# Kernel optimization log

Measured on AMD Instinct MI355X. Metric: run time of the kernel, lower is better.

Reference implementation:

```python
import jax, jax.numpy as jnp
import numpy as np

B, C, P, H, W, S = 4, 256, 128, 56, 56, 5
EPS = 1e-5


def setup_inputs() -> dict:
    key = jax.random.key(0)
    ks = jax.random.split(key, 6)
    return {
        "x": jax.random.normal(ks[0], (B, C, H, W), jnp.float32),
        "Wt": jax.random.normal(ks[1], (P, C), jnp.float32) * 0.05,
        "Wp": jax.random.normal(ks[2], (P, C), jnp.float32) * 0.05,
        "Wg": jax.random.normal(ks[3], (S, P, C), jnp.float32) * 0.05,
        "W1": jax.random.normal(ks[4], (S, C, P), jnp.float32) * 0.05,
        "W2": jax.random.normal(ks[5], (S, C, P), jnp.float32) * 0.05,
        "gamma": jnp.ones((S, C), jnp.float32),
        "beta": jnp.zeros((S, C), jnp.float32),
    }


def _batchnorm(o, g, b):
    # training-mode BN over (batch, spatial); o: [b, C, n]
    mean = o.mean(axis=(0, 2), keepdims=True)
    var = ((o - mean) ** 2).mean(axis=(0, 2), keepdims=True)
    return (o - mean) * jax.lax.rsqrt(var + EPS) * g[None, :, None] + b[None, :, None]


def reference(x, Wt, Wp, Wg, W1, W2, gamma, beta):
    b, c, h, w = x.shape
    n = h * w
    xf = x.reshape(b, c, n)
    # 1x1 conv projections == channel matmuls
    t = jax.nn.relu(jnp.einsum('pc,bcn->bpn', Wt, xf))  # is_norm branch uses relu
    p = jax.nn.relu(jnp.einsum('pc,bcn->bpn', Wp, xf))
    att = jnp.einsum('bpi,bpj->bij', t, p)              # [b, n, n] affinity
    att = 0.5 * (att + jnp.swapaxes(att, 1, 2))         # is_sys symmetrization
    d = att.sum(axis=2)                                  # degree [b, n]
    d_safe = jnp.where(d != 0, d, 1.0)
    d_inv = jnp.where(d != 0, jax.lax.rsqrt(d_safe), 0.0)
    att = att * d_inv[:, None, :] * d_inv[:, :, None]    # D^-1/2 A D^-1/2
    out = xf
    for s in range(S):  # fixed small stage count
        g = jnp.einsum('pc,bcn->bpn', Wg[s], out)        # [b, P, n]
        ag = jnp.einsum('bij,bpj->bpi', att, g)          # att @ g over spatial
        o = jnp.einsum('cp,bpn->bcn', W1[s], ag) + jnp.einsum('cp,bpn->bcn', W2[s], g)
        out = _batchnorm(o, gamma[s], beta[s]) + out     # BN + residual
    return out.reshape(b, c, h, w)
```

## Files before the change

kernel.cpp:

```cpp
#include <hip/hip_runtime.h>

#define VMC(n) asm volatile("s_waitcnt vmcnt(" #n ")" ::: "memory")

namespace {

constexpr int Bc = 4;
constexpr int Cc = 256;
constexpr int Pc = 128;
constexpr int NcT = 3136;
constexpr int Np = 3200;
constexpr int Sc = 5;
constexpr int KSn = 5;
constexpr int KCH = 640;
constexpr float EPSc = 1e-5f;

typedef __attribute__((ext_vector_type(8))) short bf16x8;
typedef __attribute__((ext_vector_type(4))) float f32x4;
typedef __attribute__((ext_vector_type(8))) unsigned short u16x8;
typedef __attribute__((ext_vector_type(4))) unsigned short u16x4;

__device__ inline float bf2f(unsigned short u) {
    return __uint_as_float(((unsigned)u) << 16);
}
__device__ inline unsigned short f2bf(float f) {
    unsigned u = __float_as_uint(f);
    return (unsigned short)((u + 0x7FFFu + ((u >> 16) & 1u)) >> 16);
}

struct GP {
    const unsigned short* A; int lda; long aB; long aSl;
    const unsigned short* Bw; int ldb; long bB; long bSl;
    const unsigned short* A2; int lda2; long aB2;
    const unsigned short* B2; int ldb2; long bB2;
    int K; int K2; int nsl; int kchunk;
    unsigned short* outSM; int ldsm; long smB; long smSlice;
    unsigned short* outCM; long cmB;
    float* ps; float* ps2;
    const float* bnsc; const float* bnsh;
    const float* dinv;
    const unsigned short* oin;
    float* resid;
};

template <int MT, int EPI, int CMOUT, bool SPLITK, int BNSTAT, bool FUSEBN,
          bool XORM, bool DUALK>
__global__ __launch_bounds__(256) void mgemm(GP p)
{
    constexpr int TBA = MT * 64 * 2;
    constexpr int TBB = 128 * 64 * 2;
    constexpr int BUF = TBA + TBB;
    constexpr int OTB = MT * 132 * 4;
    constexpr int LDSZ = (4 * BUF > OTB + 2048) ? 4 * BUF : (OTB + 2048);
    __shared__ __align__(16) char lds[LDSZ];

    int b, kstart;
    long smOff;
    if (SPLITK) {
        b = blockIdx.z & 3;
        int ks = blockIdx.z >> 2;
        kstart = ks * p.kchunk;
        smOff = (long)ks * p.smSlice;
    } else {
        b = blockIdx.z; kstart = 0; smOff = 0;
    }
    const int n0 = blockIdx.x * 128;
    const int m0 = blockIdx.y * MT;
    const int tid = threadIdx.x;
    const int w = tid >> 6, l = tid & 63;

    const unsigned short* Ab = p.A + (size_t)b * p.aB + (size_t)m0 * p.lda;
    const unsigned short* Bb = p.Bw + (size_t)b * p.bB + (size_t)n0 * p.ldb;

    const int srow8 = tid >> 3;
    const int sgran = tid & 7;
    const int sswz = (sgran ^ (srow8 & 7)) * 8;
    constexpr int AR = MT / 32;

    constexpr int WC = (MT == 128) ? 2 : 4;
    constexpr int NB = 128 / WC / 16;
    const int wr = w / WC, wc = w % WC;

    f32x4 acc[4][NB] = {};
    float fup[AR][8];

    auto stage1 = [&](int buf, int sl, int k0) {
        char* base = lds + buf * BUF;
        const unsigned short* As = Ab + (size_t)sl * p.aSl + k0 + sswz;
#pragma unroll
        for (int j = 0; j < AR; ++j)
            __builtin_amdgcn_global_load_lds(
                (const __attribute__((address_space(1))) void*)
                    (As + (size_t)(j * 32 + srow8) * p.lda),
                (__attribute__((address_space(3))) void*)(base + j * 4096 + tid * 16),
                16, 0, 0);
        const unsigned short* Bs = Bb + (size_t)sl * p.bSl + k0 + sswz;
#pragma unroll
        for (int j = 0; j < 4; ++j)
            __builtin_amdgcn_global_load_lds(
                (const __attribute__((address_space(1))) void*)
                    (Bs + (size_t)(j * 32 + srow8) * p.ldb),
                (__attribute__((address_space(3))) void*)(base + TBA + j * 4096 + tid * 16),
                16, 0, 0);
    };

    auto stageB1 = [&](int buf, int k0) {
        char* base = lds + buf * BUF + TBA;
        const unsigned short* Bs = Bb + k0 + sswz;
#pragma unroll
        for (int j = 0; j < 4; ++j)
            __builtin_amdgcn_global_load_lds(
                (const __attribute__((address_space(1))) void*)
                    (Bs + (size_t)(j * 32 + srow8) * p.ldb),
                (__attribute__((address_space(3))) void*)(base + j * 4096 + tid * 16),
                16, 0, 0);
    };

    auto fbLoad = [&](int k0) {
        const float* scp = p.bnsc + k0 + sgran * 8;
        const float* shp = p.bnsh + k0 + sgran * 8;
        float4 s0 = *(const float4*)scp, s1 = *(const float4*)(scp + 4);
        float4 h0 = *(const float4*)shp, h1 = *(const float4*)(shp + 4);
#pragma unroll
        for (int j = 0; j < AR; ++j) {
            int row = j * 32 + srow8;
            int n = m0 + row;
            size_t off = ((size_t)b * Np + n) * 256 + k0 + sgran * 8;
            if (n < NcT) {
                u16x8 ov = *(const u16x8*)(p.oin + off);
                float4 r0 = *(const float4*)(p.resid + off);
                float4 r1 = *(const float4*)(p.resid + off + 4);
                fup[j][0] = r0.x + fmaf(bf2f(ov[0]), s0.x, h0.x);
                fup[j][1] = r0.y + fmaf(bf2f(ov[1]), s0.y, h0.y);
                fup[j][2] = r0.z + fmaf(bf2f(ov[2]), s0.z, h0.z);
                fup[j][3] = r0.w + fmaf(bf2f(ov[3]), s0.w, h0.w);
                fup[j][4] = r1.x + fmaf(bf2f(ov[4]), s1.x, h1.x);
                fup[j][5] = r1.y + fmaf(bf2f(ov[5]), s1.y, h1.y);
                fup[j][6] = r1.z + fmaf(bf2f(ov[6]), s1.z, h1.z);
                fup[j][7] = r1.w + fmaf(bf2f(ov[7]), s1.w, h1.w);
                float4 w0, w1;
                w0.x = fup[j][0]; w0.y = fup[j][1]; w0.z = fup[j][2]; w0.w = fup[j][3];
                w1.x = fup[j][4]; w1.y = fup[j][5]; w1.z = fup[j][6]; w1.w = fup[j][7];
                *(float4*)(p.resid + off) = w0;
                *(float4*)(p.resid + off + 4) = w1;
            } else {
#pragma unroll
                for (int i = 0; i < 8; ++i) fup[j][i] = 0.f;
            }
        }
    };
    auto fbWrite = [&](int buf) {
        char* base = lds + buf * BUF;
#pragma unroll
        for (int j = 0; j < AR; ++j) {
            int row = j * 32 + srow8;
            u16x8 hv;
#pragma unroll
            for (int i = 0; i < 8; ++i) hv[i] = f2bf(fup[j][i]);
            *(u16x8*)(base + row * 128 + ((sgran ^ (row & 7)) << 4)) = hv;
        }
    };

    auto compute = [&](int buf) {
        const char* base = lds + buf * BUF;
        const int lo = l & 15, gq = l >> 4;
#pragma unroll
        for (int kh = 0; kh < 2; ++kh) {
            const int lg = kh * 4 + gq;
            bf16x8 bf[NB];
#pragma unroll
            for (int c = 0; c < NB; ++c) {
                int brow = wc * (16 * NB) + c * 16 + lo;
                bf[c] = *(const bf16x8*)(base + TBA + brow * 128 +
                                         ((lg ^ (brow & 7)) << 4));
            }
#pragma unroll
            for (int r = 0; r < 4; ++r) {
                int arow = wr * 64 + r * 16 + lo;
                bf16x8 af = *(const bf16x8*)(base + arow * 128 +
                                             ((lg ^ (arow & 7)) << 4));
#pragma unroll
                for (int c = 0; c < NB; ++c)
                    acc[r][c] = __builtin_amdgcn_mfma_f32_16x16x32_bf16(
                        af, bf[c], acc[r][c], 0, 0, 0);
            }
        }
    };

    if constexpr (FUSEBN) {
        const int nst = p.K >> 6;
        fbLoad(kstart);
        fbWrite(0);
        stageB1(0, kstart);
        __syncthreads();
        for (int s = 0; s < nst; ++s) {
            if (s + 1 < nst) {
                fbLoad(kstart + ((s + 1) << 6));
                stageB1((s + 1) & 1, kstart + ((s + 1) << 6));
            }
            compute(s & 1);
            if (s + 1 < nst) fbWrite((s + 1) & 1);
            __syncthreads();
        }
    } else {
        const int nsteps1 = (SPLITK ? p.kchunk : p.K) >> 6;
        const int spl2 = DUALK ? (p.K2 >> 6) : 0;
        const int loop1 = p.nsl * nsteps1;
        const int tot = loop1 + spl2;

        const unsigned short* Ab2 = DUALK ?
            (p.A2 + (size_t)b * p.aB2 + (size_t)m0 * p.lda2) : nullptr;
        const unsigned short* Bb2 = DUALK ?
            (p.B2 + (size_t)b * p.bB2 + (size_t)n0 * p.ldb2) : nullptr;
        auto stage2 = [&](int buf, int k0) {
            if constexpr (DUALK) {
                char* base = lds + buf * BUF;
                const unsigned short* As = Ab2 + k0 + sswz;
#pragma unroll
                for (int j = 0; j < AR; ++j)
                    __builtin_amdgcn_global_load_lds(
                        (const __attribute__((address_space(1))) void*)
                            (As + (size_t)(j * 32 + srow8) * p.lda2),
                        (__attribute__((address_space(3))) void*)(base + j * 4096 + tid * 16),
                        16, 0, 0);
                const unsigned short* Bs = Bb2 + k0 + sswz;
#pragma unroll
                for (int j = 0; j < 4; ++j)
                    __builtin_amdgcn_global_load_lds(
                        (const __attribute__((address_space(1))) void*)
                            (Bs + (size_t)(j * 32 + srow8) * p.ldb2),
                        (__attribute__((address_space(3))) void*)(base + TBA + j * 4096 + tid * 16),
                        16, 0, 0);
            }
        };

        auto stage_g = [&](int buf, int g) {
            if (g < loop1) {
                int sl = g / nsteps1;
                int st = g - sl * nsteps1;
                stage1(buf, sl, kstart + (st << 6));
            } else {
                stage2(buf, (g - loop1) << 6);
            }
        };

        stage_g(0, 0);
        if (1 < tot) stage_g(1, 1);
        if (2 < tot) stage_g(2, 2);
        for (int gs = 0; gs < tot; ++gs) {
            if constexpr (MT == 64) {
                if (gs + 2 < tot) VMC(12);
                else if (gs + 1 < tot) VMC(6);
                else VMC(0);
            } else {
                if (gs + 2 < tot) VMC(16);
                else if (gs + 1 < tot) VMC(8);
                else VMC(0);
            }
            __builtin_amdgcn_s_barrier();
            __builtin_amdgcn_sched_barrier(0);
            if (gs + 3 < tot) stage_g((gs + 3) & 3, gs + 3);
            compute(gs & 3);
        }
        __syncthreads();
    }

    float* ot = (float*)lds;
    {
        const int lo = l & 15, gq = l >> 4;
#pragma unroll
        for (int r = 0; r < 4; ++r)
#pragma unroll
            for (int c = 0; c < NB; ++c)
#pragma unroll
                for (int j = 0; j < 4; ++j) {
                    float v = acc[r][c][j];
                    if (EPI == 1) v = fmaxf(v, 0.f);
                    ot[(wr * 64 + r * 16 + gq * 4 + j) * 132 +
                       wc * (16 * NB) + c * 16 + lo] = v;
                }
    }
    __syncthreads();

    {
        constexpr int TPR = 256 / MT;
        const int r = tid / TPR;
        const int c0 = (tid % TPR) * (MT / 2);
        const int m0s = XORM ? (m0 ^ 128) : m0;
        unsigned short* dst = p.outSM + (size_t)b * p.smB + smOff +
                              (size_t)(m0s + r) * p.ldsm + n0 + c0;
#pragma unroll
        for (int k = 0; k < MT / 16; ++k) {
            u16x8 o;
#pragma unroll
            for (int j = 0; j < 8; ++j) o[j] = f2bf(ot[r * 132 + c0 + 8 * k + j]);
            *(u16x8*)(dst + 8 * k) = o;
        }
    }

    if (CMOUT) {
        const int c = tid >> 1, r0 = (tid & 1) * (MT / 2);
        const float* dv = p.dinv + (size_t)b * Np + m0 + r0;
        unsigned short* dst = p.outCM + (size_t)b * p.cmB +
                              (size_t)(n0 + c) * Np + m0 + r0;
#pragma unroll
        for (int k = 0; k < MT / 16; ++k) {
            u16x8 o;
#pragma unroll
            for (int j = 0; j < 8; ++j) {
                float v = ot[(r0 + 8 * k + j) * 132 + c];
                if (CMOUT == 2) v *= dv[8 * k + j];
                o[j] = f2bf(v);
            }
            *(u16x8*)(dst + 8 * k) = o;
        }
    }

    if (BNSTAT) {
        float* p1 = (float*)(lds + OTB);
        float* p2 = p1 + 256;
        const int col = tid & 127, half = tid >> 7;
        float s = 0.f, s2 = 0.f;
#pragma unroll
        for (int i = 0; i < MT / 2; ++i) {
            float v = ot[(half * (MT / 2) + i) * 132 + col];
            s += v;
            if (BNSTAT == 2) s2 = fmaf(v, v, s2);
        }
        p1[half * 128 + col] = s;
        if (BNSTAT == 2) p2[half * 128 + col] = s2;
        __syncthreads();
        if (tid < 128) {
            float aa = p1[tid] + p1[128 + tid];
            size_t slot = ((size_t)b * gridDim.y + blockIdx.y) * 256 + n0 + tid;
            p.ps[slot] = aa;
            if (BNSTAT == 2) p.ps2[slot] = p2[tid] + p2[128 + tid];
        }
    }
}

__global__ __launch_bounds__(256) void prep_k(
    const float* __restrict__ x, const float* __restrict__ Wt,
    const float* __restrict__ Wp, const float* __restrict__ Wg,
    const float* __restrict__ W1, const float* __restrict__ W2,
    unsigned short* __restrict__ Wcomb, unsigned short* __restrict__ Wgh,
    unsigned short* __restrict__ W1h, unsigned short* __restrict__ W2h,
    float* __restrict__ out_sm, unsigned short* __restrict__ outh)
{
    __shared__ float tb[64][65];
    int item = blockIdx.x;
    int t = threadIdx.x;
    if (item < 544) {
        size_t e = ((size_t)item * 256 + t) * 4;
        const float* src; unsigned short* dst;
        if (e < 32768)       { src = Wt + e;           dst = Wcomb + e; }
        else if (e < 65536)  { src = Wp + (e - 32768); dst = Wcomb + e; }
        else if (e < 229376) { size_t o = e - 65536;  src = Wg + o; dst = Wgh + o; }
        else if (e < 393216) { size_t o = e - 229376; src = W1 + o; dst = W1h + o; }
        else                 { size_t o = e - 393216; src = W2 + o; dst = W2h + o; }
        float4 v = *(const float4*)src;
        u16x4 t4;
        t4[0] = f2bf(v.x); t4[1] = f2bf(v.y); t4[2] = f2bf(v.z); t4[3] = f2bf(v.w);
        *(u16x4*)dst = t4;
        return;
    }
    int it = item - 544;
    int nx = it % 50, cy = (it / 50) % 4, b = it / 200;
    int c0 = cy * 64, n0 = nx * 64;
    const bool pad = (n0 >= NcT);
    if (!pad) {
        int ci = t >> 2, nb = (t & 3) * 16;
        const float* src = x + ((size_t)b * Cc + c0 + ci) * NcT + n0 + nb;
#pragma unroll
        for (int k = 0; k < 4; ++k) {
            float4 v = *(const float4*)(src + 4 * k);
            tb[ci][nb + 4 * k + 0] = v.x; tb[ci][nb + 4 * k + 1] = v.y;
            tb[ci][nb + 4 * k + 2] = v.z; tb[ci][nb + 4 * k + 3] = v.w;
        }
    }
    __syncthreads();
    int r = t >> 2, cb = (t & 3) * 16;
    size_t off = ((size_t)b * Np + n0 + r) * 256 + c0 + cb;
    float vv[16];
#pragma unroll
    for (int j = 0; j < 16; ++j) vv[j] = pad ? 0.f : tb[cb + j][r];
    float* dst = out_sm + off;
#pragma unroll
    for (int k = 0; k < 4; ++k) {
        float4 v; v.x = vv[4*k]; v.y = vv[4*k+1]; v.z = vv[4*k+2]; v.w = vv[4*k+3];
        *(float4*)(dst + 4 * k) = v;
    }
    u16x8 h1, h2;
#pragma unroll
    for (int j = 0; j < 8; ++j) { h1[j] = f2bf(vv[j]); h2[j] = f2bf(vv[8 + j]); }
    unsigned short* dh = outh + off;
    *(u16x8*)dh = h1;
    *(u16x8*)(dh + 8) = h2;
}

__global__ __launch_bounds__(256) void dinvud_k(
    const unsigned short* __restrict__ U, const float* __restrict__ rp,
    float* __restrict__ dinv, unsigned short* __restrict__ Ud)
{
    __shared__ float rsl[256];
    __shared__ float dl[256];
    int b = blockIdx.y, tid = threadIdx.x;
    float s = 0.f;
    for (int j = 0; j < 25; ++j) s += rp[((size_t)b * 25 + j) * 256 + tid];
    rsl[tid ^ 128] = s;
    __syncthreads();
    const int i0 = blockIdx.x * 256;
    const int i = i0 + tid;
    float dv = 0.f;
    if (i < Np) {
        const unsigned short* row = U + ((size_t)b * Np + i) * 256;
        float acc = 0.f;
        for (int q0 = 0; q0 < 256; q0 += 8) {
            u16x8 v = *(const u16x8*)(row + q0);
#pragma unroll
            for (int j = 0; j < 8; ++j) acc = fmaf(bf2f(v[j]), rsl[q0 + j], acc);
        }
        float d = 0.5f * acc;
        dv = d > 0.f ? rsqrtf(d) : 0.f;
        dinv[(size_t)b * Np + i] = dv;
    }
    dl[tid] = 0.5f * dv;
    __syncthreads();
    for (int pass = 0; pass < 32; ++pass) {
        int row = pass * 8 + (tid >> 5);
        int gi = i0 + row;
        if (gi < Np) {
            size_t off = ((size_t)b * Np + gi) * 256 + (tid & 31) * 8;
            u16x8 v = *(const u16x8*)(U + off);
            float sc = dl[row];
            u16x8 o;
#pragma unroll
            for (int j = 0; j < 8; ++j) o[j] = f2bf(bf2f(v[j]) * sc);
            *(u16x8*)(Ud + off) = o;
        }
    }
}

__global__ __launch_bounds__(256) void bnfin_k(
    const float* __restrict__ ps, const float* __restrict__ ps2,
    const float* __restrict__ gamma, const float* __restrict__ beta,
    float* __restrict__ scale, float* __restrict__ shift)
{
    __shared__ float l1[256], l2[256];
    int t = threadIdx.x;
    int c = blockIdx.x * 16 + (t & 15);
    int gl = t >> 4;
    float a = 0.f, a2 = 0.f;
    for (int g = gl; g < 100; g += 16) {
        a += ps[(size_t)g * 256 + c];
        a2 += ps2[(size_t)g * 256 + c];
    }
    l1[t] = a; l2[t] = a2;
    __syncthreads();
    if (gl == 0) {
#pragma unroll
        for (int j = 1; j < 16; ++j) {
            a += l1[j * 16 + (t & 15)];
            a2 += l2[j * 16 + (t & 15)];
        }
        const float inv = 1.f / (float)(Bc * NcT);
        float mean = a * inv;
        float var = a2 * inv - mean * mean;
        float sc = gamma[c] * rsqrtf(var + EPSc);
        scale[c] = sc;
        shift[c] = beta[c] - mean * sc;
    }
}

__global__ __launch_bounds__(256) void xpoutbn_k(
    const float* __restrict__ out_sm, const unsigned short* __restrict__ oin,
    const float* __restrict__ scale, const float* __restrict__ shift,
    float* __restrict__ outp)
{
    __shared__ float tb[64][65];
    __shared__ float lsc[64], lsh[64];
    int b = blockIdx.z, c0 = blockIdx.y * 64, n0 = blockIdx.x * 64;
    int t = threadIdx.x;
    if (t < 64) { lsc[t] = scale[c0 + t]; lsh[t] = shift[c0 + t]; }
    __syncthreads();
    {
        int r = t >> 2, cb = (t & 3) * 16;
        size_t off = ((size_t)b * Np + n0 + r) * 256 + c0 + cb;
#pragma unroll
        for (int k = 0; k < 2; ++k) {
            float4 a0 = *(const float4*)(out_sm + off + 8 * k);
            float4 a1 = *(const float4*)(out_sm + off + 8 * k + 4);
            u16x8 ov = *(const u16x8*)(oin + off + 8 * k);
            tb[r][cb + 8*k + 0] = a0.x + fmaf(bf2f(ov[0]), lsc[cb + 8*k + 0], lsh[cb + 8*k + 0]);
            tb[r][cb + 8*k + 1] = a0.y + fmaf(bf2f(ov[1]), lsc[cb + 8*k + 1], lsh[cb + 8*k + 1]);
            tb[r][cb + 8*k + 2] = a0.z + fmaf(bf2f(ov[2]), lsc[cb + 8*k + 2], lsh[cb + 8*k + 2]);
            tb[r][cb + 8*k + 3] = a0.w + fmaf(bf2f(ov[3]), lsc[cb + 8*k + 3], lsh[cb + 8*k + 3]);
            tb[r][cb + 8*k + 4] = a1.x + fmaf(bf2f(ov[4]), lsc[cb + 8*k + 4], lsh[cb + 8*k + 4]);
            tb[r][cb + 8*k + 5] = a1.y + fmaf(bf2f(ov[5]), lsc[cb + 8*k + 5], lsh[cb + 8*k + 5]);
            tb[r][cb + 8*k + 6] = a1.z + fmaf(bf2f(ov[6]), lsc[cb + 8*k + 6], lsh[cb + 8*k + 6]);
            tb[r][cb + 8*k + 7] = a1.w + fmaf(bf2f(ov[7]), lsc[cb + 8*k + 7], lsh[cb + 8*k + 7]);
        }
    }
    __syncthreads();
    {
        int c = t >> 2, rb = (t & 3) * 16;
        float vv[16];
#pragma unroll
        for (int j = 0; j < 16; ++j) vv[j] = tb[rb + j][c];
        float* dst = outp + ((size_t)b * Cc + c0 + c) * NcT + n0 + rb;
#pragma unroll
        for (int k = 0; k < 4; ++k) {
            float4 v; v.x = vv[4*k]; v.y = vv[4*k+1]; v.z = vv[4*k+2]; v.w = vv[4*k+3];
            *(float4*)(dst + 4 * k) = v;
        }
    }
}

}

extern "C" void kernel_launch(void* const* d_in, const int* in_sizes, int n_in,
                              void* d_out, int out_size, void* d_ws, size_t ws_size,
                              hipStream_t stream) {
    const float* x     = (const float*)d_in[0];
    const float* Wt    = (const float*)d_in[1];
    const float* Wp    = (const float*)d_in[2];
    const float* Wg    = (const float*)d_in[3];
    const float* W1    = (const float*)d_in[4];
    const float* W2    = (const float*)d_in[5];
    const float* gamma = (const float*)d_in[6];
    const float* beta  = (const float*)d_in[7];

    char* p = (char*)d_ws;
    auto alloc = [&](size_t bytes) { char* r = p; p += (bytes + 255) & ~(size_t)255; return r; };
    float*          out_sm = (float*)         alloc((size_t)Bc * Np * 256 * 4);
    unsigned short* outh   = (unsigned short*)alloc((size_t)Bc * Np * 256 * 2);
    unsigned short* U_sm   = (unsigned short*)alloc((size_t)Bc * Np * 256 * 2);
    unsigned short* U_cm   = (unsigned short*)alloc((size_t)Bc * 256 * Np * 2);
    unsigned short* Ud     = (unsigned short*)alloc((size_t)Bc * Np * 256 * 2);
    unsigned short* g_sm   = (unsigned short*)alloc((size_t)Bc * Np * Pc * 2);
    unsigned short* g_cmd  = (unsigned short*)alloc((size_t)Bc * Pc * Np * 2);
    unsigned short* o_sm   = (unsigned short*)alloc((size_t)Bc * Np * 256 * 2);
    unsigned short* Cpart  = (unsigned short*)alloc((size_t)KSn * Bc * 256 * Pc * 2);
    unsigned short* WMb    = (unsigned short*)alloc((size_t)Bc * Cc * 256 * 2);
    unsigned short* Wcomb  = (unsigned short*)alloc((size_t)Cc * Cc * 2);
    unsigned short* Wgh    = (unsigned short*)alloc((size_t)Sc * Pc * Cc * 2);
    unsigned short* W1h    = (unsigned short*)alloc((size_t)Sc * Cc * Pc * 2);
    unsigned short* W2h    = (unsigned short*)alloc((size_t)Sc * Cc * Pc * 2);
    float*          rp     = (float*)         alloc((size_t)100 * 256 * 4);
    float*          dinv   = (float*)         alloc((size_t)Bc * Np * 4);
    float*          ps     = (float*)         alloc((size_t)100 * 256 * 4);
    float*          ps2    = (float*)         alloc((size_t)100 * 256 * 4);
    float*          scale  = (float*)         alloc(256 * 4);
    float*          shiftb = (float*)         alloc(256 * 4);

    const long NpC = (long)Np * 256;
    dim3 blk(256);

    prep_k<<<1344, blk, 0, stream>>>(x, Wt, Wp, Wg, W1, W2,
                                     Wcomb, Wgh, W1h, W2h, out_sm, outh);

    {
        GP g{};
        g.A = outh; g.lda = 256; g.aB = NpC; g.aSl = 0;
        g.Bw = Wcomb; g.ldb = 256; g.bB = 0; g.bSl = 0;
        g.K = 256; g.nsl = 1;
        g.outSM = U_sm; g.ldsm = 256; g.smB = NpC; g.smSlice = 0;
        g.outCM = U_cm; g.cmB = (long)256 * Np;
        g.ps = rp;
        mgemm<128, 1, 1, false, 1, false, false, false>
            <<<dim3(2, 25, Bc), blk, 0, stream>>>(g);
    }

    dinvud_k<<<dim3(13, Bc), blk, 0, stream>>>(U_sm, rp, dinv, Ud);

    for (int s = 0; s < Sc; ++s) {
        {
            GP g{};
            g.A = outh; g.lda = 256; g.aB = NpC; g.aSl = 0;
            g.Bw = Wgh + (size_t)s * Pc * Cc; g.ldb = 256; g.bB = 0; g.bSl = 0;
            g.K = 256; g.nsl = 1;
            g.outSM = g_sm; g.ldsm = 128; g.smB = (long)Np * 128; g.smSlice = 0;
            g.outCM = g_cmd; g.cmB = (long)Pc * Np;
            g.dinv = dinv;
            g.oin = o_sm; g.bnsc = scale; g.bnsh = shiftb; g.resid = out_sm;
            if (s == 0)
                mgemm<64, 0, 2, false, 0, false, false, false>
                    <<<dim3(1, 50, Bc), blk, 0, stream>>>(g);
            else
                mgemm<64, 0, 2, false, 0, true, false, false>
                    <<<dim3(1, 50, Bc), blk, 0, stream>>>(g);
        }
        {
            GP g{};
            g.A = U_cm; g.lda = Np; g.aB = (long)256 * Np; g.aSl = 0;
            g.Bw = g_cmd; g.ldb = Np; g.bB = (long)Pc * Np; g.bSl = 0;
            g.K = Np; g.kchunk = KCH; g.nsl = 1;
            g.outSM = Cpart; g.ldsm = 128; g.smB = (long)256 * Pc;
            g.smSlice = (long)Bc * 256 * Pc;
            mgemm<64, 0, 0, true, 0, false, true, false>
                <<<dim3(1, 4, KSn * Bc), blk, 0, stream>>>(g);
        }
        {
            GP g{};
            g.A = W1h + (size_t)s * Cc * Pc; g.lda = 128; g.aB = 0; g.aSl = 0;
            g.Bw = Cpart; g.ldb = 128; g.bB = (long)256 * Pc;
            g.bSl = (long)Bc * 256 * Pc;
            g.K = 128; g.nsl = KSn;
            g.outSM = WMb; g.ldsm = 256; g.smB = (long)Cc * 256; g.smSlice = 0;
            mgemm<64, 0, 0, false, 0, false, false, false>
                <<<dim3(2, 4, Bc), blk, 0, stream>>>(g);
        }
        {
            GP g{};
            g.A = Ud; g.lda = 256; g.aB = NpC; g.aSl = 0;
            g.Bw = WMb; g.ldb = 256; g.bB = (long)Cc * 256; g.bSl = 0;
            g.K = 256; g.nsl = 1;
            g.A2 = g_sm; g.lda2 = 128; g.aB2 = (long)Np * 128;
            g.B2 = W2h + (size_t)s * Cc * Pc; g.ldb2 = 128; g.bB2 = 0;
            g.K2 = 128;
            g.outSM = o_sm; g.ldsm = 256; g.smB = NpC; g.smSlice = 0;
            g.ps = ps; g.ps2 = ps2;
            mgemm<128, 0, 0, false, 2, false, false, true>
                <<<dim3(2, 25, Bc), blk, 0, stream>>>(g);
        }
        bnfin_k<<<16, blk, 0, stream>>>(ps, ps2, gamma + s * Cc, beta + s * Cc,
                                        scale, shiftb);
    }

    xpoutbn_k<<<dim3(49, 4, Bc), blk, 0, stream>>>(out_sm, o_sm, scale, shiftb,
                                                   (float*)d_out);
}
```

Measured before the change: 256.9 us.

## Fold degree scaling into dual-K GEMM epilogue and deepen fused-BN prefetch pipeline

The pre-scaled Ud buffer is no longer materialised. The dinv kernel now only computes degrees, and the dual-K GEMM reads U_sm directly, multiplying its first-phase accumulators by 0.5·dinv per row before the second K phase is added. Separately, the fused BN/residual prologue of the g-projection GEMM is rewritten as an explicitly unrolled, four-buffer software pipeline with split issue/finish stages and manual vmcnt/lgkmcnt waits. The aim is to overlap the global loads with MFMA work and to cut one full-size pass over U. The unrolled schedule hardcodes K=256 and specific wait counts, which is fragile, and changes bf16 rounding (U is no longer pre-scaled before the bf16 cast).

```diff
diff --git a/kernel.cpp b/kernel.cpp
--- a/kernel.cpp
+++ b/kernel.cpp
@@ -1,6 +1,7 @@
 #include <hip/hip_runtime.h>
 
 #define VMC(n) asm volatile("s_waitcnt vmcnt(" #n ")" ::: "memory")
+#define LGKM0() asm volatile("s_waitcnt lgkmcnt(0)" ::: "memory")
 
 namespace {
 
@@ -81,7 +82,17 @@
     const int wr = w / WC, wc = w % WC;
 
     f32x4 acc[4][NB] = {};
-    float fup[AR][8];
+
+    float4 dvv[4];
+    if constexpr (DUALK) {
+#pragma unroll
+        for (int r = 0; r < 4; ++r) {
+            float4 v = *(const float4*)(p.dinv + (size_t)b * Np + m0 +
+                                        wr * 64 + r * 16 + (l >> 4) * 4);
+            v.x *= 0.5f; v.y *= 0.5f; v.z *= 0.5f; v.w *= 0.5f;
+            dvv[r] = v;
+        }
+    }
 
     auto stage1 = [&](int buf, int sl, int k0) {
         char* base = lds + buf * BUF;
@@ -115,51 +126,6 @@
                 16, 0, 0);
     };
 
-    auto fbLoad = [&](int k0) {
-        const float* scp = p.bnsc + k0 + sgran * 8;
-        const float* shp = p.bnsh + k0 + sgran * 8;
-        float4 s0 = *(const float4*)scp, s1 = *(const float4*)(scp + 4);
-        float4 h0 = *(const float4*)shp, h1 = *(const float4*)(shp + 4);
-#pragma unroll
-        for (int j = 0; j < AR; ++j) {
-            int row = j * 32 + srow8;
-            int n = m0 + row;
-            size_t off = ((size_t)b * Np + n) * 256 + k0 + sgran * 8;
-            if (n < NcT) {
-                u16x8 ov = *(const u16x8*)(p.oin + off);
-                float4 r0 = *(const float4*)(p.resid + off);
-                float4 r1 = *(const float4*)(p.resid + off + 4);
-                fup[j][0] = r0.x + fmaf(bf2f(ov[0]), s0.x, h0.x);
-                fup[j][1] = r0.y + fmaf(bf2f(ov[1]), s0.y, h0.y);
-                fup[j][2] = r0.z + fmaf(bf2f(ov[2]), s0.z, h0.z);
-                fup[j][3] = r0.w + fmaf(bf2f(ov[3]), s0.w, h0.w);
-                fup[j][4] = r1.x + fmaf(bf2f(ov[4]), s1.x, h1.x);
-                fup[j][5] = r1.y + fmaf(bf2f(ov[5]), s1.y, h1.y);
-                fup[j][6] = r1.z + fmaf(bf2f(ov[6]), s1.z, h1.z);
-                fup[j][7] = r1.w + fmaf(bf2f(ov[7]), s1.w, h1.w);
-                float4 w0, w1;
-                w0.x = fup[j][0]; w0.y = fup[j][1]; w0.z = fup[j][2]; w0.w = fup[j][3];
-                w1.x = fup[j][4]; w1.y = fup[j][5]; w1.z = fup[j][6]; w1.w = fup[j][7];
-                *(float4*)(p.resid + off) = w0;
-                *(float4*)(p.resid + off + 4) = w1;
-            } else {
-#pragma unroll
-                for (int i = 0; i < 8; ++i) fup[j][i] = 0.f;
-            }
-        }
-    };
-    auto fbWrite = [&](int buf) {
-        char* base = lds + buf * BUF;
-#pragma unroll
-        for (int j = 0; j < AR; ++j) {
-            int row = j * 32 + srow8;
-            u16x8 hv;
-#pragma unroll
-            for (int i = 0; i < 8; ++i) hv[i] = f2bf(fup[j][i]);
-            *(u16x8*)(base + row * 128 + ((sgran ^ (row & 7)) << 4)) = hv;
-        }
-    };
-
     auto compute = [&](int buf) {
         const char* base = lds + buf * BUF;
         const int lo = l & 15, gq = l >> 4;
@@ -187,20 +153,84 @@
     };
 
     if constexpr (FUSEBN) {
-        const int nst = p.K >> 6;
-        fbLoad(kstart);
-        fbWrite(0);
-        stageB1(0, kstart);
+        struct FB {
+            u16x8 ov[AR]; float4 r0[AR], r1[AR];
+            float4 s0, s1, h0, h1; int k0;
+        };
+        FB fA, fB;
+        auto fbIssue = [&](FB& f, int k0) {
+            f.k0 = k0;
+            f.s0 = *(const float4*)(p.bnsc + k0 + sgran * 8);
+            f.s1 = *(const float4*)(p.bnsc + k0 + sgran * 8 + 4);
+            f.h0 = *(const float4*)(p.bnsh + k0 + sgran * 8);
+            f.h1 = *(const float4*)(p.bnsh + k0 + sgran * 8 + 4);
+#pragma unroll
+            for (int j = 0; j < AR; ++j) {
+                size_t off = ((size_t)b * Np + (m0 + j * 32 + srow8)) * 256 +
+                             k0 + sgran * 8;
+                f.ov[j] = *(const u16x8*)(p.oin + off);
+                f.r0[j] = *(const float4*)(p.resid + off);
+                f.r1[j] = *(const float4*)(p.resid + off + 4);
+            }
+        };
+        auto fbFin = [&](FB& f, int buf) {
+            char* base = lds + buf * BUF;
+#pragma unroll
+            for (int j = 0; j < AR; ++j) {
+                int row = j * 32 + srow8;
+                int n = m0 + row;
+                size_t off = ((size_t)b * Np + n) * 256 + f.k0 + sgran * 8;
+                bool real = (n < NcT);
+                float fu[8];
+                fu[0] = real ? f.r0[j].x + fmaf(bf2f(f.ov[j][0]), f.s0.x, f.h0.x) : 0.f;
+                fu[1] = real ? f.r0[j].y + fmaf(bf2f(f.ov[j][1]), f.s0.y, f.h0.y) : 0.f;
+                fu[2] = real ? f.r0[j].z + fmaf(bf2f(f.ov[j][2]), f.s0.z, f.h0.z) : 0.f;
+                fu[3] = real ? f.r0[j].w + fmaf(bf2f(f.ov[j][3]), f.s0.w, f.h0.w) : 0.f;
+                fu[4] = real ? f.r1[j].x + fmaf(bf2f(f.ov[j][4]), f.s1.x, f.h1.x) : 0.f;
+                fu[5] = real ? f.r1[j].y + fmaf(bf2f(f.ov[j][5]), f.s1.y, f.h1.y) : 0.f;
+                fu[6] = real ? f.r1[j].z + fmaf(bf2f(f.ov[j][6]), f.s1.z, f.h1.z) : 0.f;
+                fu[7] = real ? f.r1[j].w + fmaf(bf2f(f.ov[j][7]), f.s1.w, f.h1.w) : 0.f;
+                float4 w0, w1;
+                w0.x = fu[0]; w0.y = fu[1]; w0.z = fu[2]; w0.w = fu[3];
+                w1.x = fu[4]; w1.y = fu[5]; w1.z = fu[6]; w1.w = fu[7];
+                *(float4*)(p.resid + off) = w0;
+                *(float4*)(p.resid + off + 4) = w1;
+                u16x8 hv;
+#pragma unroll
+                for (int i = 0; i < 8; ++i) hv[i] = f2bf(fu[i]);
+                *(u16x8*)(base + row * 128 + ((sgran ^ (row & 7)) << 4)) = hv;
+            }
+        };
+
+        fbIssue(fA, kstart);        stageB1(0, kstart);
+        fbIssue(fB, kstart + 64);   stageB1(1, kstart + 64);
+        VMC(14);
+        fbFin(fA, 0);
+        fbIssue(fA, kstart + 128);  stageB1(2, kstart + 128);
+        LGKM0();
+        __builtin_amdgcn_s_barrier();
+        __builtin_amdgcn_sched_barrier(0);
+        compute(0);
+        VMC(18);
+        fbFin(fB, 1);
+        fbIssue(fB, kstart + 192);  stageB1(3, kstart + 192);
+        LGKM0();
+        __builtin_amdgcn_s_barrier();
+        __builtin_amdgcn_sched_barrier(0);
+        compute(1);
+        VMC(18);
+        fbFin(fA, 2);
+        LGKM0();
+        __builtin_amdgcn_s_barrier();
+        __builtin_amdgcn_sched_barrier(0);
+        compute(2);
+        VMC(4);
+        fbFin(fB, 3);
+        LGKM0();
+        __builtin_amdgcn_s_barrier();
+        __builtin_amdgcn_sched_barrier(0);
+        compute(3);
         __syncthreads();
-        for (int s = 0; s < nst; ++s) {
-            if (s + 1 < nst) {
-                fbLoad(kstart + ((s + 1) << 6));
-                stageB1((s + 1) & 1, kstart + ((s + 1) << 6));
-            }
-            compute(s & 1);
-            if (s + 1 < nst) fbWrite((s + 1) & 1);
-            __syncthreads();
-        }
     } else {
         const int nsteps1 = (SPLITK ? p.kchunk : p.K) >> 6;
         const int spl2 = DUALK ? (p.K2 >> 6) : 0;
@@ -260,6 +290,20 @@
             __builtin_amdgcn_sched_barrier(0);
             if (gs + 3 < tot) stage_g((gs + 3) & 3, gs + 3);
             compute(gs & 3);
+            if constexpr (DUALK) {
+                if (gs == loop1 - 1) {
+#pragma unroll
+                    for (int r = 0; r < 4; ++r) {
+#pragma unroll
+                        for (int c = 0; c < NB; ++c) {
+                            acc[r][c][0] *= dvv[r].x;
+                            acc[r][c][1] *= dvv[r].y;
+                            acc[r][c][2] *= dvv[r].z;
+                            acc[r][c][3] *= dvv[r].w;
+                        }
+                    }
+                }
+            }
         }
         __syncthreads();
     }
@@ -397,20 +441,17 @@
     *(u16x8*)(dh + 8) = h2;
 }
 
-__global__ __launch_bounds__(256) void dinvud_k(
+__global__ __launch_bounds__(256) void dinv_k(
     const unsigned short* __restrict__ U, const float* __restrict__ rp,
-    float* __restrict__ dinv, unsigned short* __restrict__ Ud)
+    float* __restrict__ dinv)
 {
     __shared__ float rsl[256];
-    __shared__ float dl[256];
     int b = blockIdx.y, tid = threadIdx.x;
     float s = 0.f;
     for (int j = 0; j < 25; ++j) s += rp[((size_t)b * 25 + j) * 256 + tid];
     rsl[tid ^ 128] = s;
     __syncthreads();
-    const int i0 = blockIdx.x * 256;
-    const int i = i0 + tid;
-    float dv = 0.f;
+    int i = blockIdx.x * 256 + tid;
     if (i < Np) {
         const unsigned short* row = U + ((size_t)b * Np + i) * 256;
         float acc = 0.f;
@@ -420,23 +461,7 @@
             for (int j = 0; j < 8; ++j) acc = fmaf(bf2f(v[j]), rsl[q0 + j], acc);
         }
         float d = 0.5f * acc;
-        dv = d > 0.f ? rsqrtf(d) : 0.f;
-        dinv[(size_t)b * Np + i] = dv;
-    }
-    dl[tid] = 0.5f * dv;
-    __syncthreads();
-    for (int pass = 0; pass < 32; ++pass) {
-        int row = pass * 8 + (tid >> 5);
-        int gi = i0 + row;
-        if (gi < Np) {
-            size_t off = ((size_t)b * Np + gi) * 256 + (tid & 31) * 8;
-            u16x8 v = *(const u16x8*)(U + off);
-            float sc = dl[row];
-            u16x8 o;
-#pragma unroll
-            for (int j = 0; j < 8; ++j) o[j] = f2bf(bf2f(v[j]) * sc);
-            *(u16x8*)(Ud + off) = o;
-        }
+        dinv[(size_t)b * Np + i] = d > 0.f ? rsqrtf(d) : 0.f;
     }
 }
 
@@ -535,7 +560,6 @@
     unsigned short* outh   = (unsigned short*)alloc((size_t)Bc * Np * 256 * 2);
     unsigned short* U_sm   = (unsigned short*)alloc((size_t)Bc * Np * 256 * 2);
     unsigned short* U_cm   = (unsigned short*)alloc((size_t)Bc * 256 * Np * 2);
-    unsigned short* Ud     = (unsigned short*)alloc((size_t)Bc * Np * 256 * 2);
     unsigned short* g_sm   = (unsigned short*)alloc((size_t)Bc * Np * Pc * 2);
     unsigned short* g_cmd  = (unsigned short*)alloc((size_t)Bc * Pc * Np * 2);
     unsigned short* o_sm   = (unsigned short*)alloc((size_t)Bc * Np * 256 * 2);
@@ -570,7 +594,7 @@
             <<<dim3(2, 25, Bc), blk, 0, stream>>>(g);
     }
 
-    dinvud_k<<<dim3(13, Bc), blk, 0, stream>>>(U_sm, rp, dinv, Ud);
+    dinv_k<<<dim3(13, Bc), blk, 0, stream>>>(U_sm, rp, dinv);
 
     for (int s = 0; s < Sc; ++s) {
         {
@@ -611,7 +635,7 @@
         }
         {
             GP g{};
-            g.A = Ud; g.lda = 256; g.aB = NpC; g.aSl = 0;
+            g.A = U_sm; g.lda = 256; g.aB = NpC; g.aSl = 0;
             g.Bw = WMb; g.ldb = 256; g.bB = (long)Cc * 256; g.bSl = 0;
             g.K = 256; g.nsl = 1;
             g.A2 = g_sm; g.lda2 = 128; g.aB2 = (long)Np * 128;
@@ -619,6 +643,7 @@
             g.K2 = 128;
             g.outSM = o_sm; g.ldsm = 256; g.smB = NpC; g.smSlice = 0;
             g.ps = ps; g.ps2 = ps2;
+            g.dinv = dinv;
             mgemm<128, 0, 0, false, 2, false, false, true>
                 <<<dim3(2, 25, Bc), blk, 0, stream>>>(g);
         }
```

After: 250.5 us (median of 2 runs). 2.5% less time.
